# Kernel optimization log

Measured on AMD Instinct MI355X. Metric: run time of the kernel, lower is better.

## Reference

```python
import jax, jax.numpy as jnp
import numpy as np

B, L, D = 4, 2048, 2048
H = 16
DH = D // H           # 128
DC = 512              # d_kv_compress


def rotate_half(x):
    x1, x2 = jnp.split(x, 2, axis=-1)
    return jnp.concatenate([-x2, x1], axis=-1)


def apply_rotary_emb(x, cos, sin):
    return x * cos + rotate_half(x) * sin


def setup_inputs() -> dict:
    key = jax.random.key(0)
    ks = jax.random.split(key, 8)
    s = 1.0 / np.sqrt(D)
    sc = 1.0 / np.sqrt(DC)
    return {
        "x": jax.random.normal(ks[0], (B, L, D), jnp.float32),
        "rope_cos": jax.random.uniform(ks[1], (B, L, DH), jnp.float32),
        "rope_sin": jax.random.uniform(ks[2], (B, L, DH), jnp.float32),
        # weights stored as (out, in) like nn.Linear
        "W_q": jax.random.normal(ks[3], (D, D), jnp.float32) * s,
        "W_dkv": jax.random.normal(ks[4], (DC, D), jnp.float32) * s,
        "W_uk": jax.random.normal(ks[5], (D, DC), jnp.float32) * sc,
        "W_uv": jax.random.normal(ks[6], (D, DC), jnp.float32) * sc,
        "W_o": jax.random.normal(ks[7], (D, D), jnp.float32) * s,
    }


def reference(x, rope_cos, rope_sin, W_q, W_dkv, W_uk, W_uv, W_o):
    scale = DH ** (-0.5)
    # projections: y = x @ W.T
    Q = (x @ W_q.T).reshape(B, L, H, DH).transpose(0, 2, 1, 3)    # [B,H,L,DH]
    c_kv = x @ W_dkv.T                                            # [B,L,DC]
    K = (c_kv @ W_uk.T).reshape(B, L, H, DH).transpose(0, 2, 1, 3)
    V = (c_kv @ W_uv.T).reshape(B, L, H, DH).transpose(0, 2, 1, 3)
    cos = rope_cos[:, None, :, :]  # [B,1,L,DH]
    sin = rope_sin[:, None, :, :]
    Q = apply_rotary_emb(Q, cos, sin)
    K = apply_rotary_emb(K, cos, sin)
    # non-causal SDPA
    scores = jnp.einsum("bhqd,bhkd->bhqk", Q, K) * scale
    attn = jax.nn.softmax(scores, axis=-1)
    out = jnp.einsum("bhqk,bhkd->bhqd", attn, V)                  # [B,H,L,DH]
    out = out.transpose(0, 2, 1, 3).reshape(B, L, D)
    return out @ W_o.T
```

## Files before the change

### kernel.cpp

```cpp
#include <hip/hip_runtime.h>
#include <math.h>

typedef __attribute__((ext_vector_type(8))) short bf16x8;
typedef __attribute__((ext_vector_type(4))) float f32x4;
typedef __attribute__((ext_vector_type(16))) float f32x16;

#define NB 4
#define NL 2048
#define ND 2048
#define NH 16
#define NDH 128
#define NDC 512
#define NROWS (NB*NL)

__device__ __forceinline__ unsigned short f2bf(float f) {
  unsigned int u = __float_as_uint(f);
  u += 0x7fffu + ((u >> 16) & 1u);
  return (unsigned short)(u >> 16);
}
__device__ __forceinline__ float bf2f(unsigned short h) {
  return __uint_as_float(((unsigned int)h) << 16);
}
__device__ __forceinline__ unsigned int cvtpk(float lo, float hi) {
  unsigned int r;
  asm("v_cvt_pk_bf16_f32 %0, %1, %2" : "=v"(r) : "v"(lo), "v"(hi));
  return r;
}
__device__ __forceinline__ void permswap(unsigned int &a, unsigned int &b) {
  asm("v_permlane32_swap_b32 %0, %1" : "+v"(a), "+v"(b));
}
__device__ __forceinline__ float exp2_fast(float x) {
  float r; asm("v_exp_f32 %0, %1" : "=v"(r) : "v"(x)); return r;
}

__device__ __forceinline__ void gld16(const void* g, void* l) {
  __builtin_amdgcn_global_load_lds((const __attribute__((address_space(1))) void*)g,
                                   (__attribute__((address_space(3))) void*)l, 16, 0, 0);
}

struct Cvt6 {
  const float4* s[6];
  ushort4* d[6];
  int n4[6];
};
__global__ void cvt6_kernel(Cvt6 cv) {
  const int seg = blockIdx.y;
  const float4* __restrict__ in = cv.s[seg];
  ushort4* __restrict__ out = cv.d[seg];
  const int n4 = cv.n4[seg];
  int stride = gridDim.x * blockDim.x;
  for (int i = blockIdx.x * blockDim.x + threadIdx.x; i < n4; i += stride) {
    float4 v = in[i];
    ushort4 o;
    o.x = f2bf(v.x); o.y = f2bf(v.y); o.z = f2bf(v.z); o.w = f2bf(v.w);
    out[i] = o;
  }
}

template<int OUT_F32>
__global__ __launch_bounds__(256) void gemm_nt(const unsigned short* __restrict__ A,
                                               const unsigned short* __restrict__ Bm,
                                               void* __restrict__ Cv,
                                               int M, int N, int K) {
  __shared__ unsigned short As[128 * 32];
  __shared__ unsigned short Bs[128 * 32];
  const int tid = threadIdx.x;
  const int wid = tid >> 6;
  const int lane = tid & 63;
  const int wr = wid >> 1, wc = wid & 1;
  const long bm = blockIdx.y, bn = blockIdx.x;
  const int r15 = lane & 15;
  const int koff = (lane >> 4) * 8;
  const int srow = lane >> 2;
  const int scol = (lane & 3) * 8;

  f32x4 acc[4][4];
#pragma unroll
  for (int m = 0; m < 4; ++m)
#pragma unroll
    for (int n = 0; n < 4; ++n) acc[m][n] = (f32x4){0.f, 0.f, 0.f, 0.f};

  const unsigned short* Ablk = A + (bm * 128 + wid * 16 + srow) * (long)K + scol;
  const unsigned short* Bblk = Bm + (bn * 128 + wid * 16 + srow) * (long)K + scol;
  unsigned short* AsW = As + wid * 16 * 32;
  unsigned short* BsW = Bs + wid * 16 * 32;

  for (int kk = 0; kk < K; kk += 32) {
    __syncthreads();
#pragma unroll
    for (int j = 0; j < 2; ++j) {
      gld16(Ablk + (long)j * 64 * K + kk, AsW + j * 64 * 32);
      gld16(Bblk + (long)j * 64 * K + kk, BsW + j * 64 * 32);
    }
    __syncthreads();
    bf16x8 af[4], bfr[4];
#pragma unroll
    for (int m = 0; m < 4; ++m)
      af[m] = *(const bf16x8*)(As + (wr * 64 + m * 16 + r15) * 32 + koff);
#pragma unroll
    for (int n = 0; n < 4; ++n)
      bfr[n] = *(const bf16x8*)(Bs + (wc * 64 + n * 16 + r15) * 32 + koff);
#pragma unroll
    for (int m = 0; m < 4; ++m)
#pragma unroll
      for (int n = 0; n < 4; ++n)
        acc[m][n] = __builtin_amdgcn_mfma_f32_16x16x32_bf16(af[m], bfr[n], acc[m][n], 0, 0, 0);
  }

  const int rr = (lane >> 4) * 4;
#pragma unroll
  for (int m = 0; m < 4; ++m) {
#pragma unroll
    for (int n = 0; n < 4; ++n) {
      long row0 = bm * 128 + wr * 64 + m * 16 + rr;
      long col = bn * 128 + wc * 64 + n * 16 + r15;
#pragma unroll
      for (int r = 0; r < 4; ++r) {
        float v = acc[m][n][r];
        if (OUT_F32) ((float*)Cv)[(row0 + r) * (long)N + col] = v;
        else ((unsigned short*)Cv)[(row0 + r) * (long)N + col] = f2bf(v);
      }
    }
  }
}

template<int OUT_F32, int ROPE>
__global__ __launch_bounds__(512) void gemm_nt256(const unsigned short* __restrict__ A,
                                                  const unsigned short* __restrict__ Bm,
                                                  void* __restrict__ Cv,
                                                  int M, int N, int K,
                                                  const float* __restrict__ cosb,
                                                  const float* __restrict__ sinb,
                                                  float rscale) {
  __shared__ unsigned short lds[2][2][16384];
  const int tid = threadIdx.x;
  const int wid = tid >> 6, lane = tid & 63;
  const int wm = wid >> 2, wn = wid & 3;
  const int r15 = lane & 15, khi = lane >> 4;

  const int gx = gridDim.x;
  int bid = blockIdx.y * gx + blockIdx.x;
  int cpx = (gx * gridDim.y) >> 3;
  int swz = (bid & 7) * cpx + (bid >> 3);
  const long bm = swz / gx, bn = swz % gx;

  const int c0 = tid, c1 = 512 + tid;
  const int r0 = c0 >> 3, r1 = c1 >> 3;
  const int cs0 = ((c0 & 7) ^ (r0 & 7)) * 8;
  const int cs1 = ((c1 & 7) ^ (r1 & 7)) * 8;
  const unsigned short* srcA = A + (bm * 256) * (long)K;
  const unsigned short* srcB = Bm + (bn * 256) * (long)K;

#define STAGE256(mat, h, kb, bufi) do {                                              \
    const unsigned short* s_ = (mat) ? srcB : srcA;                                  \
    gld16(s_ + ((h) * 128 + r0) * (long)K + (kb) + cs0,                              \
          &lds[bufi][mat][(h) * 8192 + wid * 512]);                                  \
    gld16(s_ + ((h) * 128 + r1) * (long)K + (kb) + cs1,                              \
          &lds[bufi][mat][(h) * 8192 + 4096 + wid * 512]);                           \
  } while (0)

  f32x4 acc[8][4];
#pragma unroll
  for (int m = 0; m < 8; ++m)
#pragma unroll
    for (int n = 0; n < 4; ++n) acc[m][n] = (f32x4){0.f, 0.f, 0.f, 0.f};

  const int NT = K >> 6;
  STAGE256(0, 0, 0, 0); STAGE256(0, 1, 0, 0);
  STAGE256(1, 0, 0, 0); STAGE256(1, 1, 0, 0);

  for (int t = 0; t < NT; ++t) {
    const int buf = t & 1, nbuf = buf ^ 1;
    const int kb1 = (t + 1) << 6;
    const bool pf = (t + 1 < NT);
    __builtin_amdgcn_s_barrier();
    if (pf) {
      STAGE256(0, 0, kb1, nbuf);
      asm volatile("s_waitcnt vmcnt(2)" ::: "memory");
    } else {
      asm volatile("s_waitcnt vmcnt(0)" ::: "memory");
    }
    __builtin_amdgcn_s_barrier();

    bf16x8 bfr[4][2];
#pragma unroll
    for (int n = 0; n < 4; ++n)
#pragma unroll
      for (int kk = 0; kk < 2; ++kk) {
        int rb = wn * 64 + n * 16 + r15;
        bfr[n][kk] = *(const bf16x8*)&lds[buf][1][rb * 64 + (((kk * 4 + khi) ^ (rb & 7)) * 8)];
      }
#pragma unroll
    for (int mb = 0; mb < 4; ++mb) {
      if (mb != 0) {
        __builtin_amdgcn_s_barrier();
        if (pf) {
          if (mb == 1) STAGE256(0, 1, kb1, nbuf);
          else if (mb == 2) STAGE256(1, 0, kb1, nbuf);
          else STAGE256(1, 1, kb1, nbuf);
        }
      }
      bf16x8 af[2][2];
#pragma unroll
      for (int m2 = 0; m2 < 2; ++m2)
#pragma unroll
        for (int kk = 0; kk < 2; ++kk) {
          int ra = wm * 128 + mb * 32 + m2 * 16 + r15;
          af[m2][kk] = *(const bf16x8*)&lds[buf][0][ra * 64 + (((kk * 4 + khi) ^ (ra & 7)) * 8)];
        }
      asm volatile("s_waitcnt lgkmcnt(0)" ::: "memory");
      __builtin_amdgcn_sched_barrier(0);
      __builtin_amdgcn_s_setprio(1);
#pragma unroll
      for (int m2 = 0; m2 < 2; ++m2)
#pragma unroll
        for (int n = 0; n < 4; ++n)
#pragma unroll
          for (int kk = 0; kk < 2; ++kk)
            acc[mb * 2 + m2][n] = __builtin_amdgcn_mfma_f32_16x16x32_bf16(
                af[m2][kk], bfr[n][kk], acc[mb * 2 + m2][n], 0, 0, 0);
      __builtin_amdgcn_s_setprio(0);
    }
  }
#undef STAGE256

  if (!OUT_F32) {
    __syncthreads();
    unsigned short* scr = (unsigned short*)lds;
#pragma unroll
    for (int mi = 0; mi < 8; ++mi)
#pragma unroll
      for (int n = 0; n < 4; ++n) {
        int coll = wn * 64 + n * 16 + r15;
#pragma unroll
        for (int r = 0; r < 4; ++r) {
          int rowl = wm * 128 + mi * 16 + khi * 4 + r;
          scr[rowl * 256 + (coll ^ (((rowl >> 2) & 3) << 4))] = f2bf(acc[mi][n][r]);
        }
      }
    __syncthreads();
    const int d8 = (tid & 7) * 8;
#pragma unroll
    for (int j = 0; j < 8; ++j) {
      int rh = j * 64 + (tid >> 3);
      int rowl = rh >> 1, head = rh & 1;
      long grow = bm * 256 + rowl;
      int sw = ((rowl >> 2) & 3) << 4;
      int cl_ = head * 128 + d8;
      bf16x8 qlo = *(const bf16x8*)(scr + rowl * 256 + (cl_ ^ sw));
      bf16x8 qhi = *(const bf16x8*)(scr + rowl * 256 + ((cl_ + 64) ^ sw));
      bf16x8 olo, ohi;
      if (ROPE) {
        const float* cr = cosb + grow * NDH;
        const float* sr = sinb + grow * NDH;
        float4 cA = *(const float4*)(cr + d8), cB = *(const float4*)(cr + d8 + 4);
        float4 cC = *(const float4*)(cr + d8 + 64), cD = *(const float4*)(cr + d8 + 68);
        float4 sA = *(const float4*)(sr + d8), sB = *(const float4*)(sr + d8 + 4);
        float4 sC = *(const float4*)(sr + d8 + 64), sD = *(const float4*)(sr + d8 + 68);
        float clo[8] = {cA.x, cA.y, cA.z, cA.w, cB.x, cB.y, cB.z, cB.w};
        float chi[8] = {cC.x, cC.y, cC.z, cC.w, cD.x, cD.y, cD.z, cD.w};
        float slo[8] = {sA.x, sA.y, sA.z, sA.w, sB.x, sB.y, sB.z, sB.w};
        float shi[8] = {sC.x, sC.y, sC.z, sC.w, sD.x, sD.y, sD.z, sD.w};
#pragma unroll
        for (int i = 0; i < 8; ++i) {
          float q1 = bf2f((unsigned short)qlo[i]);
          float q2 = bf2f((unsigned short)qhi[i]);
          olo[i] = (short)f2bf((q1 * clo[i] - q2 * slo[i]) * rscale);
          ohi[i] = (short)f2bf((q2 * chi[i] + q1 * shi[i]) * rscale);
        }
      } else {
        olo = qlo;
        ohi = qhi;
      }
      unsigned short* op = (unsigned short*)Cv + grow * (long)N + bn * 256 + cl_;
      *(bf16x8*)op = olo;
      *(bf16x8*)(op + 64) = ohi;
    }
  } else {
    float* scr32 = (float*)lds;
#pragma unroll
    for (int pass = 0; pass < 2; ++pass) {
      __syncthreads();
      if (wm == pass) {
#pragma unroll
        for (int mi = 0; mi < 8; ++mi)
#pragma unroll
          for (int n = 0; n < 4; ++n) {
            int coll = wn * 64 + n * 16 + r15;
#pragma unroll
            for (int r = 0; r < 4; ++r) {
              int rowl = mi * 16 + khi * 4 + r;
              scr32[rowl * 256 + (coll ^ (((rowl >> 2) & 3) << 4))] = acc[mi][n][r];
            }
          }
      }
      __syncthreads();
#pragma unroll
      for (int j = 0; j < 16; ++j) {
        int rowl = j * 8 + wid;
        int sw = ((rowl >> 2) & 3) << 4;
        float4 v = *(const float4*)(scr32 + rowl * 256 + ((lane * 4) ^ sw));
        *(float4*)((float*)Cv + (bm * 256 + pass * 128 + rowl) * (long)N + bn * 256 + lane * 4) = v;
      }
    }
  }
}

__global__ __launch_bounds__(512) void flash_attn(const unsigned short* __restrict__ Qb,
                                                  const unsigned short* __restrict__ Kb,
                                                  const unsigned short* __restrict__ Vb,
                                                  unsigned short* __restrict__ Ob) {
  __shared__ unsigned short KsArr[2 * 8192];
  __shared__ unsigned int VtArr[2 * 4608];

  const int tid = threadIdx.x, wid = tid >> 6, lane = tid & 63;
  const int l31 = lane & 31, hi5 = lane >> 5;

  const int L = blockIdx.y * 8 + blockIdx.x;
  const int bh = ((L >> 6) << 3) | (L & 7);
  const int qt = (L >> 3) & 7;
  const int b = bh >> 4, h = bh & 15;
  const long rowbase = (long)b * NL;
  const int colbase = h * NDH;
  const long q0 = (long)qt * 256 + wid * 32;

  bf16x8 qf[8];
  {
    const unsigned short* qp = Qb + (rowbase + q0 + l31) * (long)ND + colbase + hi5 * 8;
#pragma unroll
    for (int kc = 0; kc < 8; ++kc) qf[kc] = *(const bf16x8*)(qp + kc * 16);
  }

  f32x16 oacc[4];
#pragma unroll
  for (int db = 0; db < 4; ++db)
#pragma unroll
    for (int i = 0; i < 16; ++i) oacc[db][i] = 0.f;
  float mrun = -1e30f, lrun = 0.f;

  const int kp = tid >> 4;
  const int c8 = (tid & 15) * 8;
  bf16x8 kreg[2], vreg[2];

#define LOAD_KV(kt_) do {                                                          \
    _Pragma("unroll") for (int j = 0; j < 2; ++j) {                                \
      const long grow = (rowbase + (kt_) * 64 + 2 * kp + j) * (long)ND + colbase + c8; \
      kreg[j] = *(const bf16x8*)(Kb + grow);                                       \
      vreg[j] = *(const bf16x8*)(Vb + grow);                                       \
    } } while (0)

#define WRITE_KV(bi) do {                                                          \
    _Pragma("unroll") for (int j = 0; j < 2; ++j) {                                \
      int row_ = 2 * kp + j;                                                       \
      *(bf16x8*)(KsArr + (bi) * 8192 + row_ * 128 + (c8 ^ ((row_ & 15) << 3))) = kreg[j]; \
    }                                                                              \
    _Pragma("unroll") for (int i = 0; i < 8; ++i) {                                \
      int d_ = c8 + i;                                                             \
      VtArr[(bi) * 4608 + d_ * 36 + 4 * ((kp >> 2) ^ ((d_ >> 3) & 7)) + (kp & 3)] = \
          (unsigned int)(unsigned short)vreg[0][i] |                               \
          ((unsigned int)(unsigned short)vreg[1][i] << 16);                        \
    } } while (0)

  LOAD_KV(0);
  WRITE_KV(0);
  __syncthreads();
  LOAD_KV(1);

  const int NT = NL / 64;
  for (int kt = 0; kt < NT; ++kt) {
    const int bf = kt & 1;
    const unsigned short* Ksb = KsArr + bf * 8192;
    const unsigned int* Vtb = VtArr + bf * 4608;

    f32x16 sacc[2];
    __builtin_amdgcn_s_setprio(1);
#pragma unroll
    for (int nb = 0; nb < 2; ++nb) {
#pragma unroll
      for (int i = 0; i < 16; ++i) sacc[nb][i] = 0.f;
#pragma unroll
      for (int kc = 0; kc < 8; ++kc) {
        int row = nb * 32 + l31;
        bf16x8 kf = *(const bf16x8*)(Ksb + row * 128 + ((kc * 16 + hi5 * 8) ^ ((row & 15) << 3)));
        sacc[nb] = __builtin_amdgcn_mfma_f32_32x32x16_bf16(kf, qf[kc], sacc[nb], 0, 0, 0);
      }
    }
    __builtin_amdgcn_s_setprio(0);

    if (kt + 1 < NT) WRITE_KV(bf ^ 1);
    if (kt + 2 < NT) LOAD_KV(kt + 2);

    float mxa[8];
#pragma unroll
    for (int i = 0; i < 8; ++i)
      mxa[i] = fmaxf(fmaxf(sacc[0][i], sacc[0][i + 8]), fmaxf(sacc[1][i], sacc[1][i + 8]));
    float mx = fmaxf(fmaxf(fmaxf(mxa[0], mxa[1]), fmaxf(mxa[2], mxa[3])),
                     fmaxf(fmaxf(mxa[4], mxa[5]), fmaxf(mxa[6], mxa[7])));
    mx = fmaxf(mx, __shfl_xor(mx, 32));
    if (!__all(mx - mrun <= 8.f)) {
      float mnew = fmaxf(mrun, mx);
      float corr = exp2_fast(mrun - mnew);
      mrun = mnew;
      lrun *= corr;
#pragma unroll
      for (int db = 0; db < 4; ++db)
#pragma unroll
        for (int i = 0; i < 16; ++i) oacc[db][i] *= corr;
    }
    float s4[4] = {0.f, 0.f, 0.f, 0.f};
#pragma unroll
    for (int nb = 0; nb < 2; ++nb)
#pragma unroll
      for (int r = 0; r < 16; ++r) {
        float e = exp2_fast(sacc[nb][r] - mrun);
        sacc[nb][r] = e;
        s4[r & 3] += e;
      }
    float s = (s4[0] + s4[1]) + (s4[2] + s4[3]);
    s += __shfl_xor(s, 32);
    lrun += s;

    union { unsigned int u[4]; bf16x8 v; } pa[2][2];
#pragma unroll
    for (int nb = 0; nb < 2; ++nb) {
      unsigned int x1 = cvtpk(sacc[nb][0], sacc[nb][1]);
      unsigned int x2 = cvtpk(sacc[nb][2], sacc[nb][3]);
      unsigned int y1 = cvtpk(sacc[nb][4], sacc[nb][5]);
      unsigned int y2 = cvtpk(sacc[nb][6], sacc[nb][7]);
      unsigned int z1 = cvtpk(sacc[nb][8], sacc[nb][9]);
      unsigned int z2 = cvtpk(sacc[nb][10], sacc[nb][11]);
      unsigned int w1 = cvtpk(sacc[nb][12], sacc[nb][13]);
      unsigned int w2 = cvtpk(sacc[nb][14], sacc[nb][15]);
      permswap(x1, y1);
      permswap(x2, y2);
      permswap(z1, w1);
      permswap(z2, w2);
      pa[nb][0].u[0] = x1; pa[nb][0].u[1] = x2; pa[nb][0].u[2] = y1; pa[nb][0].u[3] = y2;
      pa[nb][1].u[0] = z1; pa[nb][1].u[1] = z2; pa[nb][1].u[2] = w1; pa[nb][1].u[3] = w2;
    }

    __builtin_amdgcn_s_setprio(1);
#pragma unroll
    for (int db = 0; db < 4; ++db) {
      int d = db * 32 + l31;
      int dsw = (d >> 3) & 7;
#pragma unroll
      for (int nb = 0; nb < 2; ++nb)
#pragma unroll
        for (int ks = 0; ks < 2; ++ks) {
          int g = nb * 4 + ks * 2 + hi5;
          bf16x8 vf = *(const bf16x8*)(Vtb + d * 36 + 4 * (g ^ dsw));
          oacc[db] = __builtin_amdgcn_mfma_f32_32x32x16_bf16(vf, pa[nb][ks].v, oacc[db], 0, 0, 0);
        }
    }
    __builtin_amdgcn_s_setprio(0);
    __syncthreads();
  }
#undef LOAD_KV
#undef WRITE_KV

  float rinv = 1.0f / lrun;
  unsigned short* scr = (unsigned short*)VtArr + wid * 2304;
#pragma unroll
  for (int c = 0; c < 2; ++c) {
    asm volatile("s_waitcnt lgkmcnt(0)" ::: "memory");
    __builtin_amdgcn_sched_barrier(0);
#pragma unroll
    for (int dbh = 0; dbh < 2; ++dbh) {
      int db = 2 * c + dbh;
#pragma unroll
      for (int t = 0; t < 8; ++t) {
        int d_lo = dbh * 32 + ((2 * t) & 3) + 8 * (t >> 1) + 4 * hi5;
        unsigned int pv = cvtpk(oacc[db][2 * t] * rinv, oacc[db][2 * t + 1] * rinv);
        *(unsigned int*)(scr + l31 * 72 + d_lo) = pv;
      }
    }
    asm volatile("s_waitcnt lgkmcnt(0)" ::: "memory");
    __builtin_amdgcn_sched_barrier(0);
#pragma unroll
    for (int j = 0; j < 4; ++j) {
      int row = j * 8 + (lane >> 3);
      bf16x8 ov = *(const bf16x8*)(scr + row * 72 + (lane & 7) * 8);
      *(bf16x8*)(Ob + (rowbase + q0 + row) * (long)ND + colbase + c * 64 + (lane & 7) * 8) = ov;
    }
  }
}

extern "C" void kernel_launch(void* const* d_in, const int* in_sizes, int n_in,
                              void* d_out, int out_size, void* d_ws, size_t ws_size,
                              hipStream_t stream) {
  const float* x = (const float*)d_in[0];
  const float* rope_cos = (const float*)d_in[1];
  const float* rope_sin = (const float*)d_in[2];
  const float* W_q = (const float*)d_in[3];
  const float* W_dkv = (const float*)d_in[4];
  const float* W_uk = (const float*)d_in[5];
  const float* W_uv = (const float*)d_in[6];
  const float* W_o = (const float*)d_in[7];
  float* out = (float*)d_out;

  char* p = (char*)d_ws;
  unsigned short* xb = (unsigned short*)p;    p += (size_t)NROWS * ND * 2;
  unsigned short* Wqb = (unsigned short*)p;   p += (size_t)ND * ND * 2;
  unsigned short* Wdkvb = (unsigned short*)p; p += (size_t)NDC * ND * 2;
  unsigned short* Wukb = (unsigned short*)p;  p += (size_t)ND * NDC * 2;
  unsigned short* Wuvb = (unsigned short*)p;  p += (size_t)ND * NDC * 2;
  unsigned short* Wob = (unsigned short*)p;   p += (size_t)ND * ND * 2;
  unsigned short* Qb = (unsigned short*)p;    p += (size_t)NROWS * ND * 2;
  unsigned short* ckv = (unsigned short*)p;   p += (size_t)NROWS * NDC * 2;
  unsigned short* Kbf = (unsigned short*)p;   p += (size_t)NROWS * ND * 2;
  unsigned short* Vbf = (unsigned short*)p;   p += (size_t)NROWS * ND * 2;
  unsigned short* AO = (unsigned short*)p;    p += (size_t)NROWS * ND * 2;

  {
    Cvt6 cv;
    const float* ss[6] = {x, W_q, W_dkv, W_uk, W_uv, W_o};
    unsigned short* dd[6] = {xb, Wqb, Wdkvb, Wukb, Wuvb, Wob};
    long nn[6] = {(long)NROWS * ND, (long)ND * ND, (long)NDC * ND,
                  (long)ND * NDC, (long)ND * NDC, (long)ND * ND};
    for (int i = 0; i < 6; ++i) {
      cv.s[i] = (const float4*)ss[i];
      cv.d[i] = (ushort4*)dd[i];
      cv.n4[i] = (int)(nn[i] / 4);
    }
    cvt6_kernel<<<dim3(512, 6), 256, 0, stream>>>(cv);
  }

  const float scale_q = 0.08838834764831845f * 1.4426950408889634f;

  gemm_nt256<0, 1><<<dim3(ND / 256, NROWS / 256), 512, 0, stream>>>(
      xb, Wqb, Qb, NROWS, ND, ND, rope_cos, rope_sin, scale_q);
  gemm_nt<0><<<dim3(NDC / 128, NROWS / 128), 256, 0, stream>>>(xb, Wdkvb, ckv, NROWS, NDC, ND);
  gemm_nt256<0, 1><<<dim3(ND / 256, NROWS / 256), 512, 0, stream>>>(
      ckv, Wukb, Kbf, NROWS, ND, NDC, rope_cos, rope_sin, 1.0f);
  gemm_nt256<0, 0><<<dim3(ND / 256, NROWS / 256), 512, 0, stream>>>(
      ckv, Wuvb, Vbf, NROWS, ND, NDC, nullptr, nullptr, 0.f);

  flash_attn<<<dim3(8, 64), 512, 0, stream>>>(Qb, Kbf, Vbf, AO);

  gemm_nt256<1, 0><<<dim3(ND / 256, NROWS / 256), 512, 0, stream>>>(
      AO, Wob, out, NROWS, ND, ND, nullptr, nullptr, 0.f);
}
```

Before: 421.8 us.

## Merge Q and c_kv projections, and K and V up-projections, into grouped GEMM launches

Replaces the separate Q, c_kv, K and V projection launches with a grouped 256x256-tile GEMM that picks its weight matrix and output buffer from the block's column index. Q and c_kv now share one launch over x, and K and V share one launch over c_kv, with RoPE applied only to the first group. The small 128-tile gemm_nt kernel is dropped, so c_kv uses the larger tile path. This cuts launch count and tail effects from small grids. The trade-off is a runtime rope branch in place of a template flag, and a c_kv grid with only two column tiles per row block.

```diff
diff --git a/kernel.cpp b/kernel.cpp
--- a/kernel.cpp
+++ b/kernel.cpp
@@ -58,80 +58,16 @@
 }
 
 template<int OUT_F32>
-__global__ __launch_bounds__(256) void gemm_nt(const unsigned short* __restrict__ A,
-                                               const unsigned short* __restrict__ Bm,
-                                               void* __restrict__ Cv,
-                                               int M, int N, int K) {
-  __shared__ unsigned short As[128 * 32];
-  __shared__ unsigned short Bs[128 * 32];
-  const int tid = threadIdx.x;
-  const int wid = tid >> 6;
-  const int lane = tid & 63;
-  const int wr = wid >> 1, wc = wid & 1;
-  const long bm = blockIdx.y, bn = blockIdx.x;
-  const int r15 = lane & 15;
-  const int koff = (lane >> 4) * 8;
-  const int srow = lane >> 2;
-  const int scol = (lane & 3) * 8;
-
-  f32x4 acc[4][4];
-#pragma unroll
-  for (int m = 0; m < 4; ++m)
-#pragma unroll
-    for (int n = 0; n < 4; ++n) acc[m][n] = (f32x4){0.f, 0.f, 0.f, 0.f};
-
-  const unsigned short* Ablk = A + (bm * 128 + wid * 16 + srow) * (long)K + scol;
-  const unsigned short* Bblk = Bm + (bn * 128 + wid * 16 + srow) * (long)K + scol;
-  unsigned short* AsW = As + wid * 16 * 32;
-  unsigned short* BsW = Bs + wid * 16 * 32;
-
-  for (int kk = 0; kk < K; kk += 32) {
-    __syncthreads();
-#pragma unroll
-    for (int j = 0; j < 2; ++j) {
-      gld16(Ablk + (long)j * 64 * K + kk, AsW + j * 64 * 32);
-      gld16(Bblk + (long)j * 64 * K + kk, BsW + j * 64 * 32);
-    }
-    __syncthreads();
-    bf16x8 af[4], bfr[4];
-#pragma unroll
-    for (int m = 0; m < 4; ++m)
-      af[m] = *(const bf16x8*)(As + (wr * 64 + m * 16 + r15) * 32 + koff);
-#pragma unroll
-    for (int n = 0; n < 4; ++n)
-      bfr[n] = *(const bf16x8*)(Bs + (wc * 64 + n * 16 + r15) * 32 + koff);
-#pragma unroll
-    for (int m = 0; m < 4; ++m)
-#pragma unroll
-      for (int n = 0; n < 4; ++n)
-        acc[m][n] = __builtin_amdgcn_mfma_f32_16x16x32_bf16(af[m], bfr[n], acc[m][n], 0, 0, 0);
-  }
-
-  const int rr = (lane >> 4) * 4;
-#pragma unroll
-  for (int m = 0; m < 4; ++m) {
-#pragma unroll
-    for (int n = 0; n < 4; ++n) {
-      long row0 = bm * 128 + wr * 64 + m * 16 + rr;
-      long col = bn * 128 + wc * 64 + n * 16 + r15;
-#pragma unroll
-      for (int r = 0; r < 4; ++r) {
-        float v = acc[m][n][r];
-        if (OUT_F32) ((float*)Cv)[(row0 + r) * (long)N + col] = v;
-        else ((unsigned short*)Cv)[(row0 + r) * (long)N + col] = f2bf(v);
-      }
-    }
-  }
-}
-
-template<int OUT_F32, int ROPE>
-__global__ __launch_bounds__(512) void gemm_nt256(const unsigned short* __restrict__ A,
-                                                  const unsigned short* __restrict__ Bm,
-                                                  void* __restrict__ Cv,
-                                                  int M, int N, int K,
-                                                  const float* __restrict__ cosb,
-                                                  const float* __restrict__ sinb,
-                                                  float rscale) {
+__global__ __launch_bounds__(512) void gemm_nt256m(const unsigned short* __restrict__ A,
+                                                   const unsigned short* __restrict__ B1,
+                                                   const unsigned short* __restrict__ B2,
+                                                   void* __restrict__ C1,
+                                                   void* __restrict__ C2,
+                                                   int M, int N1, int N2, int K, int NSPLIT,
+                                                   int rope1,
+                                                   const float* __restrict__ cosb,
+                                                   const float* __restrict__ sinb,
+                                                   float rscale) {
   __shared__ unsigned short lds[2][2][16384];
   const int tid = threadIdx.x;
   const int wid = tid >> 6, lane = tid & 63;
@@ -144,12 +80,19 @@
   int swz = (bid & 7) * cpx + (bid >> 3);
   const long bm = swz / gx, bn = swz % gx;
 
+  const int grp = (bn >= NSPLIT);
+  const unsigned short* Bbase = grp ? B2 : B1;
+  void* Cout = grp ? C2 : C1;
+  const long Nout = grp ? N2 : N1;
+  const long gbn = grp ? (bn - NSPLIT) : bn;
+  const int do_rope = (!grp) && rope1;
+
   const int c0 = tid, c1 = 512 + tid;
   const int r0 = c0 >> 3, r1 = c1 >> 3;
   const int cs0 = ((c0 & 7) ^ (r0 & 7)) * 8;
   const int cs1 = ((c1 & 7) ^ (r1 & 7)) * 8;
   const unsigned short* srcA = A + (bm * 256) * (long)K;
-  const unsigned short* srcB = Bm + (bn * 256) * (long)K;
+  const unsigned short* srcB = Bbase + (gbn * 256) * (long)K;
 
 #define STAGE256(mat, h, kb, bufi) do {                                              \
     const unsigned short* s_ = (mat) ? srcB : srcA;                                  \
@@ -250,7 +193,7 @@
       bf16x8 qlo = *(const bf16x8*)(scr + rowl * 256 + (cl_ ^ sw));
       bf16x8 qhi = *(const bf16x8*)(scr + rowl * 256 + ((cl_ + 64) ^ sw));
       bf16x8 olo, ohi;
-      if (ROPE) {
+      if (do_rope) {
         const float* cr = cosb + grow * NDH;
         const float* sr = sinb + grow * NDH;
         float4 cA = *(const float4*)(cr + d8), cB = *(const float4*)(cr + d8 + 4);
@@ -272,7 +215,7 @@
         olo = qlo;
         ohi = qhi;
       }
-      unsigned short* op = (unsigned short*)Cv + grow * (long)N + bn * 256 + cl_;
+      unsigned short* op = (unsigned short*)Cout + grow * Nout + gbn * 256 + cl_;
       *(bf16x8*)op = olo;
       *(bf16x8*)(op + 64) = ohi;
     }
@@ -300,7 +243,7 @@
         int rowl = j * 8 + wid;
         int sw = ((rowl >> 2) & 3) << 4;
         float4 v = *(const float4*)(scr32 + rowl * 256 + ((lane * 4) ^ sw));
-        *(float4*)((float*)Cv + (bm * 256 + pass * 128 + rowl) * (long)N + bn * 256 + lane * 4) = v;
+        *(float4*)((float*)Cout + (bm * 256 + pass * 128 + rowl) * Nout + gbn * 256 + lane * 4) = v;
       }
     }
   }
@@ -528,16 +471,14 @@
 
   const float scale_q = 0.08838834764831845f * 1.4426950408889634f;
 
-  gemm_nt256<0, 1><<<dim3(ND / 256, NROWS / 256), 512, 0, stream>>>(
-      xb, Wqb, Qb, NROWS, ND, ND, rope_cos, rope_sin, scale_q);
-  gemm_nt<0><<<dim3(NDC / 128, NROWS / 128), 256, 0, stream>>>(xb, Wdkvb, ckv, NROWS, NDC, ND);
-  gemm_nt256<0, 1><<<dim3(ND / 256, NROWS / 256), 512, 0, stream>>>(
-      ckv, Wukb, Kbf, NROWS, ND, NDC, rope_cos, rope_sin, 1.0f);
-  gemm_nt256<0, 0><<<dim3(ND / 256, NROWS / 256), 512, 0, stream>>>(
-      ckv, Wuvb, Vbf, NROWS, ND, NDC, nullptr, nullptr, 0.f);
+  gemm_nt256m<0><<<dim3(10, 32), 512, 0, stream>>>(
+      xb, Wqb, Wdkvb, Qb, ckv, NROWS, ND, NDC, ND, 8, 1, rope_cos, rope_sin, scale_q);
+
+  gemm_nt256m<0><<<dim3(16, 32), 512, 0, stream>>>(
+      ckv, Wukb, Wuvb, Kbf, Vbf, NROWS, ND, ND, NDC, 8, 1, rope_cos, rope_sin, 1.0f);
 
   flash_attn<<<dim3(8, 64), 512, 0, stream>>>(Qb, Kbf, Vbf, AO);
 
-  gemm_nt256<1, 0><<<dim3(ND / 256, NROWS / 256), 512, 0, stream>>>(
-      AO, Wob, out, NROWS, ND, ND, nullptr, nullptr, 0.f);
-}
+  gemm_nt256m<1><<<dim3(8, 32), 512, 0, stream>>>(
+      AO, Wob, nullptr, out, nullptr, NROWS, ND, ND, ND, 8, 0, nullptr, nullptr, 0.f);
+}
```

Result: no change. 425.8 us (+0.9%).
